# Kernel optimization log

Measured on AMD Instinct MI355X. Metric: run time of the kernel, lower is better.

Reference implementation:

```python
import jax, jax.numpy as jnp
import numpy as np

VOCAB = 50257
WORD_DIM = 300
HIDDEN = 256
BATCH = 256   # number of trees
LEAVES = 1024  # leaves per complete binary tree (power of 2)


def setup_inputs() -> dict:
    key = jax.random.key(0)
    k_ids, k_emb, k_w1, k_b1, k_w2, k_b2 = jax.random.split(key, 6)
    word_ids = jax.random.randint(k_ids, (BATCH, LEAVES), 0, VOCAB)
    emb_table = jax.random.normal(k_emb, (VOCAB, WORD_DIM), dtype=jnp.float32) * 0.1
    W1 = jax.random.normal(k_w1, (WORD_DIM, HIDDEN), dtype=jnp.float32) * (1.0 / np.sqrt(WORD_DIM))
    b1 = jax.random.normal(k_b1, (HIDDEN,), dtype=jnp.float32) * 0.01
    W2 = jax.random.normal(k_w2, (2 * HIDDEN, HIDDEN), dtype=jnp.float32) * (1.0 / np.sqrt(2 * HIDDEN))
    b2 = jax.random.normal(k_b2, (HIDDEN,), dtype=jnp.float32) * 0.01
    return {"word_ids": word_ids, "emb_table": emb_table, "W1": W1, "b1": b1, "W2": W2, "b2": b2}


def reference(word_ids, emb_table, W1, b1, W2, b2):
    # Leaves: embedding lookup + word2hidden linear (no nonlinearity, as in source)
    h = jnp.einsum('blw,wh->blh', emb_table[word_ids], W1) + b1  # [B, L, H]
    # Internal nodes: concat(left, right) @ W2 + b2, level by level up the
    # complete binary tree. Loop count = log2(LEAVES), a small static constant.
    while h.shape[1] > 1:
        B, n, H = h.shape
        pairs = h.reshape(B, n // 2, 2 * H)  # concat of sibling states
        h = jnp.einsum('bnk,kh->bnh', pairs, W2) + b2
    return h[:, 0, :]  # root hidden state per tree: [B, H]
```

## Files before the change

kernel.cpp:

```cpp
#include <hip/hip_runtime.h>
#include <hip/hip_bf16.h>
#include <stdint.h>

#define VOCAB 50257
#define WD 300
#define KP1 320
#define MP 50432

using bf16 = __hip_bfloat16;
typedef __attribute__((ext_vector_type(4))) float f32x4;
typedef __attribute__((ext_vector_type(8))) short bf16x8;

__device__ __forceinline__ void async_load16(const void* g, void* l) {
    __builtin_amdgcn_global_load_lds(
        (const __attribute__((address_space(1))) uint32_t*)(uintptr_t)g,
        (__attribute__((address_space(3))) uint32_t*)l, 16, 0, 0);
}

__global__ void prep_w(const float* __restrict__ W1, const float* __restrict__ W2,
                       const float* __restrict__ b2,
                       bf16* __restrict__ w1t, bf16* __restrict__ w2t,
                       bf16* __restrict__ w2b, float* __restrict__ b4,
                       float* __restrict__ zbuf) {
    if (blockIdx.x == 1344) {
        __shared__ float b2s[256];
        int n = threadIdx.x;
        b2s[n] = b2[n];
        zbuf[n] = 0.0f;
        __syncthreads();
        float acc = b2s[n];
        #pragma unroll 8
        for (int k = 0; k < 256; ++k)
            acc += b2s[k] * (W2[k * 256 + n] + W2[(k + 256) * 256 + n]);
        b4[n] = acc;
        return;
    }
    int idx = blockIdx.x * 256 + threadIdx.x;
    if (idx < 256 * KP1) {
        int n = idx / KP1;
        int k = idx - n * KP1;
        w1t[idx] = __float2bfloat16(k < WD ? W1[k * 256 + n] : 0.0f);
    } else if (idx < 256 * KP1 + 131072) {
        int j = idx - 256 * KP1;
        int n = j >> 9, k = j & 511;
        w2t[j] = __float2bfloat16(W2[k * 256 + n]);
    } else {
        int j = idx - 256 * KP1 - 131072;
        w2b[j] = __float2bfloat16(W2[j]);
    }
}

template <int AMODE, bool OUT_F32>
__device__ __forceinline__ void tile_gemm(
    char* smem, const void* Av, const int* ids,
    const bf16* BT, int Bstr, const float* bias,
    void* C, int Cs, int coff, int K, int As, int m0,
    const float* zbuf)
{
    constexpr int ASZ = (AMODE == 2) ? 16384 : 8192;
    constexpr int BSZ = 16384, STAGE = ASZ + BSZ;

    const int t = threadIdx.x, w = t >> 6, lane = t & 63;
    const int rg = w >> 2, cgr = w & 3, mi = lane & 15, q = lane >> 4;
    const bf16* Ab = (const bf16*)Av;

    int4 idq = {0, 0, 0, 0};
    if constexpr (AMODE == 1) idq = ((const int4*)ids)[m0 + (t >> 2)];

    auto stage = [&](int ke, int buf) {
        char* Asm = smem + buf * STAGE;
        char* Bsm = Asm + ASZ;
        if constexpr (AMODE == 2) {
            const float* A32 = (const float*)Av;
            #pragma unroll
            for (int i = 0; i < 2; ++i) {
                int s = i * 512 + t;
                int row = s >> 3;
                int kcd = (s & 7) ^ (row & 7);
                int k = ke + kcd * 4;
                int grow = m0 + row; if (grow >= VOCAB) grow = VOCAB - 1;
                const float* g = (k <= 296) ? (A32 + (size_t)grow * WD + k) : zbuf;
                async_load16(g, Asm + i * 8192 + w * 1024);
            }
        } else {
            int row = t >> 2;
            int kcd = (t & 3) ^ ((row >> 2) & 3);
            const bf16* g;
            if constexpr (AMODE == 1) {
                int sel = ke >> 8;
                int id = (sel & 2) ? ((sel & 1) ? idq.w : idq.z)
                                   : ((sel & 1) ? idq.y : idq.x);
                g = Ab + (size_t)id * 256 + (ke & 255) + kcd * 8;
            } else {
                g = Ab + (size_t)(m0 + row) * As + ke + kcd * 8;
            }
            async_load16(g, Asm + w * 1024);
        }
        #pragma unroll
        for (int i = 0; i < 2; ++i) {
            int s = i * 512 + t;
            int col = s >> 2;
            int kcd = (s & 3) ^ ((col >> 2) & 3);
            async_load16(BT + (size_t)col * Bstr + ke + kcd * 8,
                         Bsm + i * 8192 + w * 1024);
        }
    };

    f32x4 acc[4][4] = {};

    auto compute = [&](int buf) {
        const char* Asm = smem + buf * STAGE;
        const bf16* Bs16 = (const bf16*)(Asm + ASZ);
        bf16x8 af[4], bfr[4];
        if constexpr (AMODE == 2) {
            const float* As32 = (const float*)Asm;
            #pragma unroll
            for (int r = 0; r < 4; ++r) {
                int row = rg * 64 + r * 16 + mi;
                int sl = row * 8 + ((2 * q) ^ (row & 7));
                f32x4 lo = *(const f32x4*)(As32 + sl * 4);
                f32x4 hi = *(const f32x4*)(As32 + (sl ^ 1) * 4);
                union { bf16x8 v; bf16 hh[8]; } u;
                #pragma unroll
                for (int j = 0; j < 4; ++j) u.hh[j] = __float2bfloat16(lo[j]);
                #pragma unroll
                for (int j = 0; j < 4; ++j) u.hh[4 + j] = __float2bfloat16(hi[j]);
                af[r] = u.v;
            }
        } else {
            const bf16* As16 = (const bf16*)Asm;
            #pragma unroll
            for (int r = 0; r < 4; ++r) {
                int row = rg * 64 + r * 16 + mi;
                int slot = row * 4 + (q ^ ((row >> 2) & 3));
                af[r] = *(const bf16x8*)(As16 + slot * 8);
            }
        }
        #pragma unroll
        for (int c = 0; c < 4; ++c) {
            int col = cgr * 64 + c * 16 + mi;
            int slot = col * 4 + (q ^ ((col >> 2) & 3));
            bfr[c] = *(const bf16x8*)(Bs16 + slot * 8);
        }
        #pragma unroll
        for (int r = 0; r < 4; ++r)
            #pragma unroll
            for (int c = 0; c < 4; ++c)
                acc[r][c] = __builtin_amdgcn_mfma_f32_16x16x32_bf16(af[r], bfr[c], acc[r][c], 0, 0, 0);
    };

    const int S = K >> 5;
    if constexpr (AMODE == 2) {
        stage(0, 0);
        for (int k0 = 0; k0 < S; ++k0) {
            if (k0 + 1 < S) {
                stage((k0 + 1) * 32, (k0 + 1) & 1);
                asm volatile("s_waitcnt vmcnt(4)\n\ts_barrier" ::: "memory");
            } else {
                asm volatile("s_waitcnt vmcnt(0)\n\ts_barrier" ::: "memory");
            }
            compute(k0 & 1);
            asm volatile("s_waitcnt lgkmcnt(0)\n\ts_barrier" ::: "memory");
        }
    } else {
        stage(0, 0);
        if (S > 1) stage(32, 1);
        for (int k0 = 0; k0 < S; ++k0) {
            if (k0 + 1 < S)
                asm volatile("s_waitcnt vmcnt(3)\n\ts_barrier" ::: "memory");
            else
                asm volatile("s_waitcnt vmcnt(0)\n\ts_barrier" ::: "memory");
            if (k0 + 2 < S) stage((k0 + 2) * 32, (k0 + 2) % 3);
            compute(k0 % 3);
        }
    }

    #pragma unroll
    for (int r = 0; r < 4; ++r) {
        int rowb = m0 + rg * 64 + r * 16 + q * 4;
        #pragma unroll
        for (int c = 0; c < 4; ++c) {
            int col = cgr * 64 + c * 16 + mi;
            float bv = bias[col];
            #pragma unroll
            for (int i = 0; i < 4; ++i) {
                float v = acc[r][c][i] + bv;
                size_t o = (size_t)(rowb + i) * Cs + coff + col;
                if (OUT_F32) ((float*)C)[o] = v;
                else         ((bf16*)C)[o] = __float2bfloat16(v);
            }
        }
    }
}

__global__ __launch_bounds__(512)
void combo(const float* __restrict__ emb, const bf16* __restrict__ w1t,
           const float* __restrict__ b1, const bf16* __restrict__ w2t,
           const bf16* __restrict__ w2b, bf16* __restrict__ w4t,
           bf16* __restrict__ proj, const float* __restrict__ zbuf) {
    __shared__ char smem[73728];
    int blk = blockIdx.x;
    if (blk < 8) {
        int j = blk >> 1, s = blk & 1;
        tile_gemm<0, false>(smem, w2t + 256 * (j >> 1), nullptr,
                            w2b + 65536 * (j & 1), 256, zbuf,
                            w4t, 1024, 256 * j, 256, 512, s * 128, nullptr);
    } else {
        tile_gemm<2, false>(smem, emb, nullptr, w1t, KP1, b1,
                            proj, 256, 0, KP1, WD, (blk - 8) * 128, zbuf);
    }
}

__global__ __launch_bounds__(512)
void mainK(const bf16* __restrict__ proj, const int* __restrict__ ids,
           const bf16* __restrict__ w4t, const float* __restrict__ b4,
           bf16* __restrict__ h) {
    __shared__ char smem[73728];
    tile_gemm<1, false>(smem, proj, ids, w4t, 1024, b4,
                        h, 256, 0, 1024, 256, blockIdx.x * 128, nullptr);
}

__global__ __launch_bounds__(512)
void treeK(const bf16* __restrict__ h, const bf16* __restrict__ w4t,
           const float* __restrict__ b4, float* __restrict__ out) {
    constexpr int ASZ = 8192, BSZ = 16384, STAGE = ASZ + BSZ;
    __shared__ char smem[3 * STAGE];
    __shared__ bf16 Ht[128 * 256];
    __shared__ bf16 Ht2[32 * 256];
    __shared__ bf16 Ht3[8 * 256];

    const int t = threadIdx.x, w = t >> 6, lane = t & 63;
    const int rg = w >> 2, cgr = w & 3, mi = lane & 15, q = lane >> 4;
    const int b = blockIdx.x;
    const int m0 = b * 128;

    {
        auto stageA = [&](int ke, int buf) {
            char* Asm = smem + buf * STAGE;
            char* Bsm = Asm + ASZ;
            int row = t >> 2;
            int kcd = (t & 3) ^ ((row >> 2) & 3);
            async_load16(h + (size_t)(m0 + row) * 1024 + ke + kcd * 8, Asm + w * 1024);
            #pragma unroll
            for (int i = 0; i < 2; ++i) {
                int s = i * 512 + t;
                int col = s >> 2;
                int kcd2 = (s & 3) ^ ((col >> 2) & 3);
                async_load16(w4t + (size_t)col * 1024 + ke + kcd2 * 8,
                             Bsm + i * 8192 + w * 1024);
            }
        };
        f32x4 acc[4][4] = {};
        stageA(0, 0); stageA(32, 1);
        for (int k0i = 0; k0i < 32; ++k0i) {
            if (k0i + 1 < 32)
                asm volatile("s_waitcnt vmcnt(3)\n\ts_barrier" ::: "memory");
            else
                asm volatile("s_waitcnt vmcnt(0)\n\ts_barrier" ::: "memory");
            if (k0i + 2 < 32) stageA((k0i + 2) * 32, (k0i + 2) % 3);
            const bf16* As16 = (const bf16*)(smem + (k0i % 3) * STAGE);
            const bf16* Bs16 = (const bf16*)(smem + (k0i % 3) * STAGE + ASZ);
            bf16x8 af[4], bfr[4];
            #pragma unroll
            for (int r = 0; r < 4; ++r) {
                int row = rg * 64 + r * 16 + mi;
                int slot = row * 4 + (q ^ ((row >> 2) & 3));
                af[r] = *(const bf16x8*)(As16 + slot * 8);
            }
            #pragma unroll
            for (int c = 0; c < 4; ++c) {
                int col = cgr * 64 + c * 16 + mi;
                int slot = col * 4 + (q ^ ((col >> 2) & 3));
                bfr[c] = *(const bf16x8*)(Bs16 + slot * 8);
            }
            #pragma unroll
            for (int r = 0; r < 4; ++r)
                #pragma unroll
                for (int c = 0; c < 4; ++c)
                    acc[r][c] = __builtin_amdgcn_mfma_f32_16x16x32_bf16(af[r], bfr[c], acc[r][c], 0, 0, 0);
        }
        #pragma unroll
        for (int r = 0; r < 4; ++r) {
            int rowb = rg * 64 + r * 16 + q * 4;
            #pragma unroll
            for (int c = 0; c < 4; ++c) {
                int col = cgr * 64 + c * 16 + mi;
                float bv = b4[col];
                int chunk = col >> 3;
                #pragma unroll
                for (int i = 0; i < 4; ++i) {
                    int row = rowb + i;
                    Ht[(row * 32 + (chunk ^ (row & 31))) * 8 + (col & 7)] =
                        __float2bfloat16(acc[r][c][i] + bv);
                }
            }
        }
    }
    __syncthreads();

    const int c0w = w * 32;
    const bf16* Bg0 = w4t + (size_t)(c0w + mi) * 1024 + q * 8;
    const bf16* Bg1 = w4t + (size_t)(c0w + 16 + mi) * 1024 + q * 8;

    {
        f32x4 acc[2][2] = {};
        #pragma unroll 4
        for (int ks = 0; ks < 32; ++ks) {
            bf16x8 b0 = *(const bf16x8*)(Bg0 + ks * 32);
            bf16x8 b1 = *(const bf16x8*)(Bg1 + ks * 32);
            int kc = (ks & 7) * 4 + q;
            int r2a = 4 * mi + (ks >> 3);
            int r2b = 4 * (16 + mi) + (ks >> 3);
            bf16x8 a0 = *(const bf16x8*)(Ht + (r2a * 32 + (kc ^ (r2a & 31))) * 8);
            bf16x8 a1 = *(const bf16x8*)(Ht + (r2b * 32 + (kc ^ (r2b & 31))) * 8);
            acc[0][0] = __builtin_amdgcn_mfma_f32_16x16x32_bf16(a0, b0, acc[0][0], 0, 0, 0);
            acc[0][1] = __builtin_amdgcn_mfma_f32_16x16x32_bf16(a0, b1, acc[0][1], 0, 0, 0);
            acc[1][0] = __builtin_amdgcn_mfma_f32_16x16x32_bf16(a1, b0, acc[1][0], 0, 0, 0);
            acc[1][1] = __builtin_amdgcn_mfma_f32_16x16x32_bf16(a1, b1, acc[1][1], 0, 0, 0);
        }
        #pragma unroll
        for (int f = 0; f < 2; ++f) {
            #pragma unroll
            for (int g = 0; g < 2; ++g) {
                int col = c0w + g * 16 + mi;
                float bv = b4[col];
                int chunk = col >> 3;
                #pragma unroll
                for (int i = 0; i < 4; ++i) {
                    int row = f * 16 + q * 4 + i;
                    Ht2[(row * 32 + (chunk ^ (row & 31))) * 8 + (col & 7)] =
                        __float2bfloat16(acc[f][g][i] + bv);
                }
            }
        }
    }
    __syncthreads();

    {
        f32x4 acc[2] = {};
        #pragma unroll 4
        for (int ks = 0; ks < 32; ++ks) {
            bf16x8 b0 = *(const bf16x8*)(Bg0 + ks * 32);
            bf16x8 b1 = *(const bf16x8*)(Bg1 + ks * 32);
            int kc = (ks & 7) * 4 + q;
            int r3 = (4 * mi + (ks >> 3)) & 31;
            bf16x8 a = *(const bf16x8*)(Ht2 + (r3 * 32 + (kc ^ (r3 & 31))) * 8);
            acc[0] = __builtin_amdgcn_mfma_f32_16x16x32_bf16(a, b0, acc[0], 0, 0, 0);
            acc[1] = __builtin_amdgcn_mfma_f32_16x16x32_bf16(a, b1, acc[1], 0, 0, 0);
        }
        if (q < 2) {
            #pragma unroll
            for (int g = 0; g < 2; ++g) {
                int col = c0w + g * 16 + mi;
                float bv = b4[col];
                #pragma unroll
                for (int i = 0; i < 4; ++i)
                    Ht3[(q * 4 + i) * 256 + col] = __float2bfloat16(acc[g][i] + bv);
            }
        }
    }
    __syncthreads();

    {
        f32x4 acc[2] = {};
        #pragma unroll 4
        for (int ks = 0; ks < 32; ++ks) {
            bf16x8 b0 = *(const bf16x8*)(Bg0 + ks * 32);
            bf16x8 b1 = *(const bf16x8*)(Bg1 + ks * 32);
            int r4 = (4 * (mi & 1) + (ks >> 3)) & 7;
            bf16x8 a = *(const bf16x8*)(Ht3 + r4 * 256 + (ks & 7) * 32 + q * 8);
            acc[0] = __builtin_amdgcn_mfma_f32_16x16x32_bf16(a, b0, acc[0], 0, 0, 0);
            acc[1] = __builtin_amdgcn_mfma_f32_16x16x32_bf16(a, b1, acc[1], 0, 0, 0);
        }
        if (q == 0) {
            #pragma unroll
            for (int g = 0; g < 2; ++g) {
                int col = c0w + g * 16 + mi;
                float bv = b4[col];
                #pragma unroll
                for (int i = 0; i < 2; ++i)
                    out[(size_t)(b * 2 + i) * 256 + col] = acc[g][i] + bv;
            }
        }
    }
}

extern "C" void kernel_launch(void* const* d_in, const int* in_sizes, int n_in,
                              void* d_out, int out_size, void* d_ws, size_t ws_size,
                              hipStream_t stream) {
    const int*   ids = (const int*)d_in[0];
    const float* emb = (const float*)d_in[1];
    const float* W1  = (const float*)d_in[2];
    const float* b1  = (const float*)d_in[3];
    const float* W2  = (const float*)d_in[4];
    const float* b2  = (const float*)d_in[5];
    (void)in_sizes; (void)n_in; (void)out_size; (void)ws_size;

    char* ws = (char*)d_ws;
    size_t off = 0;
    float* zbuf = (float*)(ws + off); off += 1024;
    float* b4   = (float*)(ws + off); off += 1024;
    bf16* w1t = (bf16*)(ws + off); off += (size_t)256 * KP1 * 2;
    bf16* w2t = (bf16*)(ws + off); off += (size_t)256 * 512 * 2;
    bf16* w2b = (bf16*)(ws + off); off += (size_t)512 * 256 * 2;
    bf16* w4t = (bf16*)(ws + off); off += (size_t)256 * 1024 * 2;
    bf16* proj = (bf16*)(ws + off); off += (size_t)MP * 256 * 2;
    bf16* h  = (bf16*)(ws + off); off += (size_t)65536 * 256 * 2;
    (void)off;

    prep_w<<<1345, 256, 0, stream>>>(W1, W2, b2, w1t, w2t, w2b, b4, zbuf);

    combo<<<402, 512, 0, stream>>>(emb, w1t, b1, w2t, w2b, w4t, proj, zbuf);

    mainK<<<512, 512, 0, stream>>>(proj, ids, w4t, b4, h);

    treeK<<<128, 512, 0, stream>>>(h, w4t, b4, (float*)d_out);
}
```

Measured before the change: 237.4 us.

## Split tree reduction to one tree per block with pre-swizzled W4 fragments

The tree kernel now launches 256 blocks, each handling a single tree's 64 rows instead of two trees' 128 rows. The first GEMM becomes a double-buffered pipeline with K-step 64, and each wave covers 32 output columns. Extra blocks added to mainK copy w4t into a fragment-ordered layout (w4c), so the later small-level GEMMs read B operands as coalesced per-lane 16-byte loads. The aim is better occupancy across CUs for the latency-bound tail, at the cost of each block re-reading the full weight matrix and an extra workspace copy.

```diff
diff --git a/kernel.cpp b/kernel.cpp
--- a/kernel.cpp
+++ b/kernel.cpp
@@ -213,123 +213,106 @@
 
 __global__ __launch_bounds__(512)
 void mainK(const bf16* __restrict__ proj, const int* __restrict__ ids,
-           const bf16* __restrict__ w4t, const float* __restrict__ b4,
-           bf16* __restrict__ h) {
+           const bf16* __restrict__ w4t, bf16* __restrict__ w4c,
+           const float* __restrict__ b4, bf16* __restrict__ h) {
     __shared__ char smem[73728];
+    if (blockIdx.x >= 512) {
+        const int tid = (blockIdx.x - 512) * 512 + threadIdx.x;
+        #pragma unroll
+        for (int i = 0; i < 8; ++i) {
+            int u = i * 4096 + tid;
+            int ln = u & 63, ks = (u >> 6) & 31, cg = u >> 11;
+            int mi2 = ln & 15, q2 = ln >> 4;
+            *(int4*)(w4c + (size_t)u * 8) =
+                *(const int4*)(w4t + (size_t)(cg * 16 + mi2) * 1024 + ks * 32 + q2 * 8);
+        }
+        return;
+    }
     tile_gemm<1, false>(smem, proj, ids, w4t, 1024, b4,
                         h, 256, 0, 1024, 256, blockIdx.x * 128, nullptr);
 }
 
 __global__ __launch_bounds__(512)
 void treeK(const bf16* __restrict__ h, const bf16* __restrict__ w4t,
-           const float* __restrict__ b4, float* __restrict__ out) {
-    constexpr int ASZ = 8192, BSZ = 16384, STAGE = ASZ + BSZ;
-    __shared__ char smem[3 * STAGE];
-    __shared__ bf16 Ht[128 * 256];
-    __shared__ bf16 Ht2[32 * 256];
-    __shared__ bf16 Ht3[8 * 256];
+           const bf16* __restrict__ w4c, const float* __restrict__ b4,
+           float* __restrict__ out) {
+    constexpr int ASZ = 8192, BSZ = 32768, STAGE = ASZ + BSZ;
+    __shared__ char smem[2 * STAGE];
+    __shared__ bf16 Ht[64 * 256];
+    __shared__ bf16 Ht2[16 * 256];
+    __shared__ bf16 Ht3[4 * 256];
 
     const int t = threadIdx.x, w = t >> 6, lane = t & 63;
-    const int rg = w >> 2, cgr = w & 3, mi = lane & 15, q = lane >> 4;
+    const int mi = lane & 15, q = lane >> 4;
     const int b = blockIdx.x;
-    const int m0 = b * 128;
 
     {
-        auto stageA = [&](int ke, int buf) {
-            char* Asm = smem + buf * STAGE;
-            char* Bsm = Asm + ASZ;
-            int row = t >> 2;
-            int kcd = (t & 3) ^ ((row >> 2) & 3);
-            async_load16(h + (size_t)(m0 + row) * 1024 + ke + kcd * 8, Asm + w * 1024);
-            #pragma unroll
-            for (int i = 0; i < 2; ++i) {
-                int s = i * 512 + t;
-                int col = s >> 2;
-                int kcd2 = (s & 3) ^ ((col >> 2) & 3);
-                async_load16(w4t + (size_t)col * 1024 + ke + kcd2 * 8,
-                             Bsm + i * 8192 + w * 1024);
-            }
+        auto stage = [&](int r, int buf) {
+            char* As = smem + buf * STAGE;
+            char* Bs = As + ASZ;
+            const int kb = r * 64;
+            {
+                int row = t >> 3, c = t & 7;
+                async_load16(h + (size_t)(64 * b + row) * 1024 + kb + ((c ^ (row & 7)) << 3),
+                             As + w * 1024);
+            }
+            #pragma unroll
+            for (int sub = 0; sub < 2; ++sub)
+                #pragma unroll
+                for (int i = 0; i < 2; ++i) {
+                    int s = i * 512 + t;
+                    int col = s >> 2;
+                    int kcd = (s & 3) ^ ((col >> 2) & 3);
+                    async_load16(w4t + (size_t)col * 1024 + kb + sub * 32 + kcd * 8,
+                                 Bs + sub * 16384 + i * 8192 + w * 1024);
+                }
         };
-        f32x4 acc[4][4] = {};
-        stageA(0, 0); stageA(32, 1);
-        for (int k0i = 0; k0i < 32; ++k0i) {
-            if (k0i + 1 < 32)
-                asm volatile("s_waitcnt vmcnt(3)\n\ts_barrier" ::: "memory");
-            else
+        f32x4 acc[4][2] = {};
+        stage(0, 0);
+        for (int r = 0; r < 16; ++r) {
+            if (r + 1 < 16) {
+                stage(r + 1, (r + 1) & 1);
+                asm volatile("s_waitcnt vmcnt(5)\n\ts_barrier" ::: "memory");
+            } else {
                 asm volatile("s_waitcnt vmcnt(0)\n\ts_barrier" ::: "memory");
-            if (k0i + 2 < 32) stageA((k0i + 2) * 32, (k0i + 2) % 3);
-            const bf16* As16 = (const bf16*)(smem + (k0i % 3) * STAGE);
-            const bf16* Bs16 = (const bf16*)(smem + (k0i % 3) * STAGE + ASZ);
-            bf16x8 af[4], bfr[4];
-            #pragma unroll
-            for (int r = 0; r < 4; ++r) {
-                int row = rg * 64 + r * 16 + mi;
-                int slot = row * 4 + (q ^ ((row >> 2) & 3));
-                af[r] = *(const bf16x8*)(As16 + slot * 8);
-            }
-            #pragma unroll
-            for (int c = 0; c < 4; ++c) {
-                int col = cgr * 64 + c * 16 + mi;
-                int slot = col * 4 + (q ^ ((col >> 2) & 3));
-                bfr[c] = *(const bf16x8*)(Bs16 + slot * 8);
-            }
-            #pragma unroll
-            for (int r = 0; r < 4; ++r)
-                #pragma unroll
-                for (int c = 0; c < 4; ++c)
-                    acc[r][c] = __builtin_amdgcn_mfma_f32_16x16x32_bf16(af[r], bfr[c], acc[r][c], 0, 0, 0);
-        }
-        #pragma unroll
-        for (int r = 0; r < 4; ++r) {
-            int rowb = rg * 64 + r * 16 + q * 4;
-            #pragma unroll
-            for (int c = 0; c < 4; ++c) {
-                int col = cgr * 64 + c * 16 + mi;
+            }
+            const bf16* As16 = (const bf16*)(smem + (r & 1) * STAGE);
+            const bf16* Bb   = (const bf16*)(smem + (r & 1) * STAGE + ASZ);
+            #pragma unroll
+            for (int kk = 0; kk < 2; ++kk) {
+                bf16x8 af[4], bfr[2];
+                #pragma unroll
+                for (int ri = 0; ri < 4; ++ri) {
+                    int row = ri * 16 + mi;
+                    int c = kk * 4 + q;
+                    af[ri] = *(const bf16x8*)(As16 + (row * 8 + (c ^ (row & 7))) * 8);
+                }
+                #pragma unroll
+                for (int c4 = 0; c4 < 2; ++c4) {
+                    int col = w * 32 + c4 * 16 + mi;
+                    int slot = col * 4 + (q ^ ((col >> 2) & 3));
+                    bfr[c4] = *(const bf16x8*)(Bb + kk * 8192 + slot * 8);
+                }
+                #pragma unroll
+                for (int ri = 0; ri < 4; ++ri)
+                    #pragma unroll
+                    for (int c4 = 0; c4 < 2; ++c4)
+                        acc[ri][c4] = __builtin_amdgcn_mfma_f32_16x16x32_bf16(af[ri], bfr[c4], acc[ri][c4], 0, 0, 0);
+            }
+            asm volatile("s_waitcnt lgkmcnt(0)\n\ts_barrier" ::: "memory");
+        }
+        #pragma unroll
+        for (int ri = 0; ri < 4; ++ri) {
+            #pragma unroll
+            for (int c4 = 0; c4 < 2; ++c4) {
+                int col = w * 32 + c4 * 16 + mi;
                 float bv = b4[col];
                 int chunk = col >> 3;
                 #pragma unroll
                 for (int i = 0; i < 4; ++i) {
-                    int row = rowb + i;
+                    int row = ri * 16 + q * 4 + i;
                     Ht[(row * 32 + (chunk ^ (row & 31))) * 8 + (col & 7)] =
-                        __float2bfloat16(acc[r][c][i] + bv);
-                }
-            }
-        }
-    }
-    __syncthreads();
-
-    const int c0w = w * 32;
-    const bf16* Bg0 = w4t + (size_t)(c0w + mi) * 1024 + q * 8;
-    const bf16* Bg1 = w4t + (size_t)(c0w + 16 + mi) * 1024 + q * 8;
-
-    {
-        f32x4 acc[2][2] = {};
-        #pragma unroll 4
-        for (int ks = 0; ks < 32; ++ks) {
-            bf16x8 b0 = *(const bf16x8*)(Bg0 + ks * 32);
-            bf16x8 b1 = *(const bf16x8*)(Bg1 + ks * 32);
-            int kc = (ks & 7) * 4 + q;
-            int r2a = 4 * mi + (ks >> 3);
-            int r2b = 4 * (16 + mi) + (ks >> 3);
-            bf16x8 a0 = *(const bf16x8*)(Ht + (r2a * 32 + (kc ^ (r2a & 31))) * 8);
-            bf16x8 a1 = *(const bf16x8*)(Ht + (r2b * 32 + (kc ^ (r2b & 31))) * 8);
-            acc[0][0] = __builtin_amdgcn_mfma_f32_16x16x32_bf16(a0, b0, acc[0][0], 0, 0, 0);
-            acc[0][1] = __builtin_amdgcn_mfma_f32_16x16x32_bf16(a0, b1, acc[0][1], 0, 0, 0);
-            acc[1][0] = __builtin_amdgcn_mfma_f32_16x16x32_bf16(a1, b0, acc[1][0], 0, 0, 0);
-            acc[1][1] = __builtin_amdgcn_mfma_f32_16x16x32_bf16(a1, b1, acc[1][1], 0, 0, 0);
-        }
-        #pragma unroll
-        for (int f = 0; f < 2; ++f) {
-            #pragma unroll
-            for (int g = 0; g < 2; ++g) {
-                int col = c0w + g * 16 + mi;
-                float bv = b4[col];
-                int chunk = col >> 3;
-                #pragma unroll
-                for (int i = 0; i < 4; ++i) {
-                    int row = f * 16 + q * 4 + i;
-                    Ht2[(row * 32 + (chunk ^ (row & 31))) * 8 + (col & 7)] =
-                        __float2bfloat16(acc[f][g][i] + bv);
+                        __float2bfloat16(acc[ri][c4][i] + bv);
                 }
             }
         }
@@ -338,24 +321,27 @@
 
     {
         f32x4 acc[2] = {};
-        #pragma unroll 4
+        #pragma unroll 8
         for (int ks = 0; ks < 32; ++ks) {
-            bf16x8 b0 = *(const bf16x8*)(Bg0 + ks * 32);
-            bf16x8 b1 = *(const bf16x8*)(Bg1 + ks * 32);
             int kc = (ks & 7) * 4 + q;
-            int r3 = (4 * mi + (ks >> 3)) & 31;
-            bf16x8 a = *(const bf16x8*)(Ht2 + (r3 * 32 + (kc ^ (r3 & 31))) * 8);
-            acc[0] = __builtin_amdgcn_mfma_f32_16x16x32_bf16(a, b0, acc[0], 0, 0, 0);
-            acc[1] = __builtin_amdgcn_mfma_f32_16x16x32_bf16(a, b1, acc[1], 0, 0, 0);
-        }
-        if (q < 2) {
+            int r2 = 4 * mi + (ks >> 3);
+            bf16x8 a = *(const bf16x8*)(Ht + (r2 * 32 + (kc ^ (r2 & 31))) * 8);
             #pragma unroll
             for (int g = 0; g < 2; ++g) {
-                int col = c0w + g * 16 + mi;
-                float bv = b4[col];
-                #pragma unroll
-                for (int i = 0; i < 4; ++i)
-                    Ht3[(q * 4 + i) * 256 + col] = __float2bfloat16(acc[g][i] + bv);
+                bf16x8 bb = *(const bf16x8*)(w4c + ((size_t)((2 * w + g) * 32 + ks) * 64 + lane) * 8);
+                acc[g] = __builtin_amdgcn_mfma_f32_16x16x32_bf16(a, bb, acc[g], 0, 0, 0);
+            }
+        }
+        #pragma unroll
+        for (int g = 0; g < 2; ++g) {
+            int col = w * 32 + g * 16 + mi;
+            float bv = b4[col];
+            int chunk = col >> 3;
+            #pragma unroll
+            for (int i = 0; i < 4; ++i) {
+                int row = q * 4 + i;
+                Ht2[(row * 32 + (chunk ^ (row & 15))) * 8 + (col & 7)] =
+                    __float2bfloat16(acc[g][i] + bv);
             }
         }
     }
@@ -363,23 +349,47 @@
 
     {
         f32x4 acc[2] = {};
-        #pragma unroll 4
+        #pragma unroll 8
         for (int ks = 0; ks < 32; ++ks) {
-            bf16x8 b0 = *(const bf16x8*)(Bg0 + ks * 32);
-            bf16x8 b1 = *(const bf16x8*)(Bg1 + ks * 32);
-            int r4 = (4 * (mi & 1) + (ks >> 3)) & 7;
+            int kc = (ks & 7) * 4 + q;
+            int r3 = (4 * mi + (ks >> 3)) & 15;
+            bf16x8 a = *(const bf16x8*)(Ht2 + (r3 * 32 + (kc ^ (r3 & 15))) * 8);
+            #pragma unroll
+            for (int g = 0; g < 2; ++g) {
+                bf16x8 bb = *(const bf16x8*)(w4c + ((size_t)((2 * w + g) * 32 + ks) * 64 + lane) * 8);
+                acc[g] = __builtin_amdgcn_mfma_f32_16x16x32_bf16(a, bb, acc[g], 0, 0, 0);
+            }
+        }
+        if (q == 0) {
+            #pragma unroll
+            for (int g = 0; g < 2; ++g) {
+                int col = w * 32 + g * 16 + mi;
+                float bv = b4[col];
+                #pragma unroll
+                for (int i = 0; i < 4; ++i)
+                    Ht3[i * 256 + col] = __float2bfloat16(acc[g][i] + bv);
+            }
+        }
+    }
+    __syncthreads();
+
+    {
+        f32x4 acc[2] = {};
+        #pragma unroll 8
+        for (int ks = 0; ks < 32; ++ks) {
+            int r4 = (4 * mi + (ks >> 3)) & 3;
             bf16x8 a = *(const bf16x8*)(Ht3 + r4 * 256 + (ks & 7) * 32 + q * 8);
-            acc[0] = __builtin_amdgcn_mfma_f32_16x16x32_bf16(a, b0, acc[0], 0, 0, 0);
-            acc[1] = __builtin_amdgcn_mfma_f32_16x16x32_bf16(a, b1, acc[1], 0, 0, 0);
+            #pragma unroll
+            for (int g = 0; g < 2; ++g) {
+                bf16x8 bb = *(const bf16x8*)(w4c + ((size_t)((2 * w + g) * 32 + ks) * 64 + lane) * 8);
+                acc[g] = __builtin_amdgcn_mfma_f32_16x16x32_bf16(a, bb, acc[g], 0, 0, 0);
+            }
         }
         if (q == 0) {
             #pragma unroll
             for (int g = 0; g < 2; ++g) {
-                int col = c0w + g * 16 + mi;
-                float bv = b4[col];
-                #pragma unroll
-                for (int i = 0; i < 2; ++i)
-                    out[(size_t)(b * 2 + i) * 256 + col] = acc[g][i] + bv;
+                int col = w * 32 + g * 16 + mi;
+                out[(size_t)b * 256 + col] = acc[g][0] + b4[col];
             }
         }
     }
@@ -404,6 +414,7 @@
     bf16* w2t = (bf16*)(ws + off); off += (size_t)256 * 512 * 2;
     bf16* w2b = (bf16*)(ws + off); off += (size_t)512 * 256 * 2;
     bf16* w4t = (bf16*)(ws + off); off += (size_t)256 * 1024 * 2;
+    bf16* w4c = (bf16*)(ws + off); off += (size_t)256 * 1024 * 2;
     bf16* proj = (bf16*)(ws + off); off += (size_t)MP * 256 * 2;
     bf16* h  = (bf16*)(ws + off); off += (size_t)65536 * 256 * 2;
     (void)off;
@@ -412,7 +423,7 @@
 
     combo<<<402, 512, 0, stream>>>(emb, w1t, b1, w2t, w2b, w4t, proj, zbuf);
 
-    mainK<<<512, 512, 0, stream>>>(proj, ids, w4t, b4, h);
-
-    treeK<<<128, 512, 0, stream>>>(h, w4t, b4, (float*)d_out);
-}
+    mainK<<<520, 512, 0, stream>>>(proj, ids, w4t, w4c, b4, h);
+
+    treeK<<<256, 512, 0, stream>>>(h, w4t, w4c, b4, (float*)d_out);
+}
```

After: 200.1 us. 1.19x faster.
